# Performance work log

Hardware: AMD Instinct MI355X
Metric: run time of the kernel (lower is better)

## Reference

```python
import jax, jax.numpy as jnp
import numpy as np

B, L, N, D = 16, 4096, 512, 256
EPS = 1e-8  # torch F.cosine_similarity default eps


def setup_inputs() -> dict:
    key = jax.random.key(0)
    k1, k2, k3 = jax.random.split(key, 3)
    spk_decoder_out = jax.random.normal(k1, (B, L, D), dtype=jnp.float32)
    profile = jax.random.normal(k2, (B, N, D), dtype=jnp.float32)
    # lengths in [1, N] so every batch has at least one valid profile
    profile_lens = jax.random.randint(k3, (B,), 1, N + 1, dtype=jnp.int32)
    return {"spk_decoder_out": spk_decoder_out, "profile": profile,
            "profile_lens": profile_lens}


def reference(spk_decoder_out, profile, profile_lens):
    # cosine similarity between (B,L,1,D) and (B,1,N,D) along D, computed
    # without materializing the (B,L,N,D) broadcast intermediate
    dots = jnp.einsum('bld,bnd->bln', spk_decoder_out, profile)      # (B,L,N)
    x_norm = jnp.sqrt(jnp.sum(spk_decoder_out * spk_decoder_out, axis=-1))  # (B,L)
    p_norm = jnp.sqrt(jnp.sum(profile * profile, axis=-1))           # (B,N)
    denom = jnp.maximum(x_norm[:, :, None] * p_norm[:, None, :], EPS)
    sim = dots / denom                                               # (B,L,N)

    # pad mask over profiles: True where n >= profile_lens[b]
    n = profile.shape[1]
    mask = jnp.arange(n, dtype=profile_lens.dtype)[None, :] >= profile_lens[:, None]  # (B,N)
    min_value = jnp.finfo(jnp.float32).min
    sim = jnp.where(mask[:, None, :], min_value, sim)
    weights = jax.nn.softmax(sim, axis=-1)
    weights = jnp.where(mask[:, None, :], 0.0, weights)              # (B,L,N)

    spk_embedding = jnp.einsum('bln,bnd->bld', weights, profile)     # (B,L,D)
    return spk_embedding, weights
```

## Files before the change

kernel.cpp:

```cpp
#include <hip/hip_runtime.h>
#include <hip/hip_bf16.h>
#include <math.h>

#define BB 16
#define LL 4096
#define NN 512
#define DD 256

typedef __attribute__((ext_vector_type(8))) short  bf16x8;
typedef __attribute__((ext_vector_type(4))) float  f32x4;
typedef __attribute__((ext_vector_type(4))) unsigned short u16x4;
typedef __attribute__((ext_vector_type(8))) unsigned short u16x8;

typedef __attribute__((address_space(1))) const void  gvoid_t;
typedef __attribute__((address_space(3))) void        lvoid_t;

#define GLL16(src, dst) __builtin_amdgcn_global_load_lds((gvoid_t*)(src), (lvoid_t*)(dst), 16, 0, 0)

__device__ __forceinline__ unsigned short f2bf(float x) {
    union { float f; unsigned u; } v; v.f = x;
    unsigned r = v.u + 0x7fffu + ((v.u >> 16) & 1u);
    return (unsigned short)(r >> 16);
}
__device__ __forceinline__ float bfhi(unsigned u) { return __uint_as_float(u & 0xffff0000u); }
__device__ __forceinline__ float bflo(unsigned u) { return __uint_as_float(u << 16); }

__global__ __launch_bounds__(256) void cda_prep(
    const float* __restrict__ P, char* __restrict__ pnI, char* __restrict__ peI)
{
    __shared__ __align__(16) char raw[16384];

    const int blk = blockIdx.x;
    const int b   = blk >> 4;
    const int c   = blk & 15;
    const int tid = threadIdx.x;
    const int nl  = tid >> 3;
    const int sub = tid & 7;

    const float* rowp = P + (((size_t)b * NN + c * 32 + nl) * DD + sub * 32);
    float4 v[8];
    #pragma unroll
    for (int k = 0; k < 8; ++k) v[k] = *(const float4*)(rowp + k * 4);

    float ss = 0.f;
    #pragma unroll
    for (int k = 0; k < 8; ++k)
        ss += v[k].x * v[k].x + v[k].y * v[k].y + v[k].z * v[k].z + v[k].w * v[k].w;
    ss += __shfl_xor(ss, 1); ss += __shfl_xor(ss, 2); ss += __shfl_xor(ss, 4);
    const float rinv = 1.0f / sqrtf(ss);

    const size_t tile = ((size_t)b * 16 + c) * 16384;

    #pragma unroll
    for (int g = 0; g < 4; ++g) {
        u16x8 h;
        #pragma unroll
        for (int j = 0; j < 8; ++j) {
            const int dl = g * 8 + j;
            const float f = ((const float*)&v[dl >> 2])[dl & 3];
            h[j] = f2bf(f * rinv);
        }
        *(u16x8*)(pnI + tile + sub * 2048 + (nl >> 4) * 1024 + (g * 16 + (nl & 15)) * 16) = h;
    }

    #pragma unroll
    for (int g = 0; g < 4; ++g) {
        u16x8 h;
        #pragma unroll
        for (int j = 0; j < 8; ++j) {
            const int dl = g * 8 + j;
            h[j] = f2bf(((const float*)&v[dl >> 2])[dl & 3]);
        }
        *(u16x8*)(raw + ((nl * 512 + sub * 64 + g * 16) ^ ((nl & 7) << 4))) = h;
    }
    __syncthreads();

    unsigned short arr[32];
    #pragma unroll
    for (int r = 0; r < 32; ++r)
        arr[r] = *(const unsigned short*)(raw + ((r * 512 + tid * 2) ^ ((r & 7) << 4)));
    #pragma unroll
    for (int g = 0; g < 4; ++g) {
        u16x8 h;
        #pragma unroll
        for (int j = 0; j < 8; ++j)
            h[j] = arr[g * 4 + (j & 3) + 16 * (j >> 2)];
        *(u16x8*)(peI + tile + (tid >> 4) * 1024 + (g * 16 + (tid & 15)) * 16) = h;
    }
}

__global__ __launch_bounds__(256, 2) void cda_main(
    const float* __restrict__ X, const char* __restrict__ pnI,
    const char* __restrict__ peI, const int* __restrict__ lens,
    float* __restrict__ out)
{
    __shared__ __align__(16) char stg[65536];

    const int id = blockIdx.x;
    const int b  = (id & 7) * 2 + (id >> 9);
    const int l0 = ((id >> 3) & 63) * 64;

    const int tid  = threadIdx.x;
    const int w    = tid >> 6;
    const int lane = tid & 63;
    const int lo   = lane & 15;
    const int g    = lane >> 4;
    const int len  = lens[b];

    const float* Xb  = X + ((size_t)b * LL + l0) * DD;
    const char*  pnB = pnI + (size_t)b * 262144;
    const char*  peB = peI + (size_t)b * 262144;

    #pragma unroll
    for (int q = 0; q < 4; ++q)
        GLL16(pnB + q * 4096 + tid * 16, stg + q * 4096 + tid * 16);

    float xinv = 0.f;
    #pragma unroll
    for (int rr = 0; rr < 16; ++rr) {
        const int row = w * 16 + rr;
        const float4 v = *(const float4*)(Xb + row * DD + lane * 4);
        float ss = v.x * v.x + v.y * v.y + v.z * v.z + v.w * v.w;
        #pragma unroll
        for (int off = 32; off > 0; off >>= 1) ss += __shfl_xor(ss, off);
        const float inv = 1.0f / sqrtf(ss);
        if (rr == lo) xinv = inv;
        u16x4 h; h.x = f2bf(v.x); h.y = f2bf(v.y); h.z = f2bf(v.z); h.w = f2bf(v.w);
        *(u16x4*)(stg + 16384 + ((row * 512 + lane * 8) ^ ((row & 7) << 4))) = h;
    }
    __syncthreads();
    bf16x8 xf[8];
    #pragma unroll
    for (int ks = 0; ks < 8; ++ks)
        xf[ks] = *(const bf16x8*)(stg + 16384 +
            (((w * 16 + lo) * 512 + ks * 64 + g * 16) ^ ((lo & 7) << 4)));
    __syncthreads();

    #pragma unroll
    for (int q = 0; q < 4; ++q)
        GLL16(pnB + 16384 + q * 4096 + tid * 16, stg + 16384 + q * 4096 + tid * 16);
    #pragma unroll
    for (int q = 0; q < 4; ++q)
        GLL16(pnB + 32768 + q * 4096 + tid * 16, stg + 32768 + q * 4096 + tid * 16);

    unsigned pm[16][4];
    float ssum = 0.f;

    #pragma unroll
    for (int c = 0; c < 16; ++c) {
        asm volatile("s_waitcnt vmcnt(8)" ::: "memory");
        __builtin_amdgcn_s_barrier();
        __builtin_amdgcn_sched_barrier(0);
        {
            const char* src = (c < 13) ? (pnB + (c + 3) * 16384)
                                       : (peB + (c - 13) * 16384);
            char* dst = stg + ((c + 3) & 3) * 16384;
            #pragma unroll
            for (int q = 0; q < 4; ++q)
                GLL16(src + q * 4096 + tid * 16, dst + q * 4096 + tid * 16);
        }
        const char* pnL = stg + (c & 3) * 16384;
        f32x4 a0 = (f32x4){0.f, 0.f, 0.f, 0.f};
        f32x4 a1 = (f32x4){0.f, 0.f, 0.f, 0.f};
        #pragma unroll
        for (int ks = 0; ks < 8; ++ks) {
            const bf16x8 f0 = *(const bf16x8*)(pnL + ks * 2048 + lane * 16);
            const bf16x8 f1 = *(const bf16x8*)(pnL + ks * 2048 + 1024 + lane * 16);
            a0 = __builtin_amdgcn_mfma_f32_16x16x32_bf16(f0, xf[ks], a0, 0, 0, 0);
            a1 = __builtin_amdgcn_mfma_f32_16x16x32_bf16(f1, xf[ks], a1, 0, 0, 0);
        }
        unsigned short pw[8];
        #pragma unroll
        for (int r = 0; r < 4; ++r) {
            const int n0 = c * 32 + g * 4 + r;
            const float p0 = (n0 < len) ? __expf(a0[r] * xinv) : 0.f;
            ssum += p0; pw[r] = f2bf(p0);
            const float p1 = (n0 + 16 < len) ? __expf(a1[r] * xinv) : 0.f;
            ssum += p1; pw[4 + r] = f2bf(p1);
        }
        pm[c][0] = (unsigned)pw[0] | ((unsigned)pw[1] << 16);
        pm[c][1] = (unsigned)pw[2] | ((unsigned)pw[3] << 16);
        pm[c][2] = (unsigned)pw[4] | ((unsigned)pw[5] << 16);
        pm[c][3] = (unsigned)pw[6] | ((unsigned)pw[7] << 16);
    }

    ssum += __shfl_xor(ssum, 16);
    ssum += __shfl_xor(ssum, 32);
    const float sinv = 1.0f / ssum;

    f32x4 e[16];
    #pragma unroll
    for (int i = 0; i < 16; ++i) e[i] = (f32x4){0.f, 0.f, 0.f, 0.f};

    float* Wrow = out + (size_t)BB * LL * DD
                + ((size_t)b * LL + l0 + w * 16 + lo) * (size_t)NN;

    #pragma unroll
    for (int c = 0; c < 16; ++c) {
        if      (c == 0) asm volatile("s_waitcnt vmcnt(8)"  ::: "memory");
        else if (c == 1) asm volatile("s_waitcnt vmcnt(10)" ::: "memory");
        else if (c <= 13) asm volatile("s_waitcnt vmcnt(12)" ::: "memory");
        else if (c == 14) asm volatile("s_waitcnt vmcnt(8)"  ::: "memory");
        else             asm volatile("s_waitcnt vmcnt(4)"  ::: "memory");
        __builtin_amdgcn_s_barrier();
        __builtin_amdgcn_sched_barrier(0);
        if (c < 13) {
            const char* src = peB + (c + 3) * 16384;
            char* dst = stg + ((c + 3) & 3) * 16384;
            #pragma unroll
            for (int q = 0; q < 4; ++q)
                GLL16(src + q * 4096 + tid * 16, dst + q * 4096 + tid * 16);
        }
        float4 v0, v1;
        v0.x = bflo(pm[c][0]) * sinv; v0.y = bfhi(pm[c][0]) * sinv;
        v0.z = bflo(pm[c][1]) * sinv; v0.w = bfhi(pm[c][1]) * sinv;
        v1.x = bflo(pm[c][2]) * sinv; v1.y = bfhi(pm[c][2]) * sinv;
        v1.z = bflo(pm[c][3]) * sinv; v1.w = bfhi(pm[c][3]) * sinv;
        *(float4*)(Wrow + c * 32 + g * 4)      = v0;
        *(float4*)(Wrow + c * 32 + 16 + g * 4) = v1;

        union { unsigned u[4]; bf16x8 v; } pf;
        pf.u[0] = pm[c][0]; pf.u[1] = pm[c][1];
        pf.u[2] = pm[c][2]; pf.u[3] = pm[c][3];
        const char* peL = stg + (c & 3) * 16384;
        #pragma unroll
        for (int df = 0; df < 16; ++df) {
            const bf16x8 bf = *(const bf16x8*)(peL + df * 1024 + lane * 16);
            e[df] = __builtin_amdgcn_mfma_f32_16x16x32_bf16(pf.v, bf, e[df], 0, 0, 0);
        }
    }
    __syncthreads();

    float t4[4];
    #pragma unroll
    for (int r = 0; r < 4; ++r) t4[r] = __shfl(sinv, g * 4 + r);
    char* scr = stg + w * 16384;
    float* Eout = out + ((size_t)b * LL + l0 + w * 16) * DD;
    #pragma unroll
    for (int r = 0; r < 4; ++r) {
        #pragma unroll
        for (int df = 0; df < 16; ++df)
            *(float*)(scr + g * 1056 + df * 64 + lo * 4) = e[df][r] * t4[r];
        #pragma unroll
        for (int it = 0; it < 4; ++it) {
            const float4 t = *(const float4*)(scr + it * 1056 + lane * 16);
            *(float4*)(Eout + (size_t)(it * 4 + r) * DD + lane * 4) = t;
        }
    }
}

extern "C" void kernel_launch(void* const* d_in, const int* in_sizes, int n_in,
                              void* d_out, int out_size, void* d_ws, size_t ws_size,
                              hipStream_t stream) {
    const float* X    = (const float*)d_in[0];
    const float* P    = (const float*)d_in[1];
    const int*   lens = (const int*)d_in[2];
    float*       out  = (float*)d_out;

    char* pnI = (char*)d_ws;
    char* peI = (char*)d_ws + 4194304;

    hipLaunchKernelGGL(cda_prep, dim3(BB * 16), dim3(256), 0, stream, P, pnI, peI);
    hipLaunchKernelGGL(cda_main, dim3(1024), dim3(256), 0, stream, X, pnI, peI, lens, out);
}
```

Baseline: 82.05 us.

## Software-pipeline softmax exp behind next chunk MFMAs, add setprio and nontemporal stores

The exp/convert work for chunk c-1 of the similarity scores now runs after the MFMAs for chunk c are issued, so the transcendental ALU work can overlap matrix-core latency. MFMA blocks are wrapped in s_setprio raises so waves doing matrix math get issue priority. Output stores for weights and embeddings switch to nontemporal stores to avoid polluting cache with write-once data. This holds an extra pair of accumulators live, which raises register pressure.

```diff
diff --git a/kernel.cpp b/kernel.cpp
--- a/kernel.cpp
+++ b/kernel.cpp
@@ -146,6 +146,8 @@
     unsigned pm[16][4];
     float ssum = 0.f;
 
+    f32x4 a0p = (f32x4){0.f, 0.f, 0.f, 0.f};
+    f32x4 a1p = (f32x4){0.f, 0.f, 0.f, 0.f};
     #pragma unroll
     for (int c = 0; c < 16; ++c) {
         asm volatile("s_waitcnt vmcnt(8)" ::: "memory");
@@ -162,6 +164,7 @@
         const char* pnL = stg + (c & 3) * 16384;
         f32x4 a0 = (f32x4){0.f, 0.f, 0.f, 0.f};
         f32x4 a1 = (f32x4){0.f, 0.f, 0.f, 0.f};
+        __builtin_amdgcn_s_setprio(1);
         #pragma unroll
         for (int ks = 0; ks < 8; ++ks) {
             const bf16x8 f0 = *(const bf16x8*)(pnL + ks * 2048 + lane * 16);
@@ -169,19 +172,39 @@
             a0 = __builtin_amdgcn_mfma_f32_16x16x32_bf16(f0, xf[ks], a0, 0, 0, 0);
             a1 = __builtin_amdgcn_mfma_f32_16x16x32_bf16(f1, xf[ks], a1, 0, 0, 0);
         }
+        __builtin_amdgcn_s_setprio(0);
+        if (c > 0) {
+            const int cp = c - 1;
+            unsigned short pw[8];
+            #pragma unroll
+            for (int r = 0; r < 4; ++r) {
+                const int n0 = cp * 32 + g * 4 + r;
+                const float p0 = (n0 < len) ? __expf(a0p[r] * xinv) : 0.f;
+                ssum += p0; pw[r] = f2bf(p0);
+                const float p1 = (n0 + 16 < len) ? __expf(a1p[r] * xinv) : 0.f;
+                ssum += p1; pw[4 + r] = f2bf(p1);
+            }
+            pm[cp][0] = (unsigned)pw[0] | ((unsigned)pw[1] << 16);
+            pm[cp][1] = (unsigned)pw[2] | ((unsigned)pw[3] << 16);
+            pm[cp][2] = (unsigned)pw[4] | ((unsigned)pw[5] << 16);
+            pm[cp][3] = (unsigned)pw[6] | ((unsigned)pw[7] << 16);
+        }
+        a0p = a0; a1p = a1;
+    }
+    {
         unsigned short pw[8];
         #pragma unroll
         for (int r = 0; r < 4; ++r) {
-            const int n0 = c * 32 + g * 4 + r;
-            const float p0 = (n0 < len) ? __expf(a0[r] * xinv) : 0.f;
+            const int n0 = 15 * 32 + g * 4 + r;
+            const float p0 = (n0 < len) ? __expf(a0p[r] * xinv) : 0.f;
             ssum += p0; pw[r] = f2bf(p0);
-            const float p1 = (n0 + 16 < len) ? __expf(a1[r] * xinv) : 0.f;
+            const float p1 = (n0 + 16 < len) ? __expf(a1p[r] * xinv) : 0.f;
             ssum += p1; pw[4 + r] = f2bf(p1);
         }
-        pm[c][0] = (unsigned)pw[0] | ((unsigned)pw[1] << 16);
-        pm[c][1] = (unsigned)pw[2] | ((unsigned)pw[3] << 16);
-        pm[c][2] = (unsigned)pw[4] | ((unsigned)pw[5] << 16);
-        pm[c][3] = (unsigned)pw[6] | ((unsigned)pw[7] << 16);
+        pm[15][0] = (unsigned)pw[0] | ((unsigned)pw[1] << 16);
+        pm[15][1] = (unsigned)pw[2] | ((unsigned)pw[3] << 16);
+        pm[15][2] = (unsigned)pw[4] | ((unsigned)pw[5] << 16);
+        pm[15][3] = (unsigned)pw[6] | ((unsigned)pw[7] << 16);
     }
 
     ssum += __shfl_xor(ssum, 16);
@@ -211,23 +234,25 @@
             for (int q = 0; q < 4; ++q)
                 GLL16(src + q * 4096 + tid * 16, dst + q * 4096 + tid * 16);
         }
-        float4 v0, v1;
-        v0.x = bflo(pm[c][0]) * sinv; v0.y = bfhi(pm[c][0]) * sinv;
-        v0.z = bflo(pm[c][1]) * sinv; v0.w = bfhi(pm[c][1]) * sinv;
-        v1.x = bflo(pm[c][2]) * sinv; v1.y = bfhi(pm[c][2]) * sinv;
-        v1.z = bflo(pm[c][3]) * sinv; v1.w = bfhi(pm[c][3]) * sinv;
-        *(float4*)(Wrow + c * 32 + g * 4)      = v0;
-        *(float4*)(Wrow + c * 32 + 16 + g * 4) = v1;
+        f32x4 v0, v1;
+        v0[0] = bflo(pm[c][0]) * sinv; v0[1] = bfhi(pm[c][0]) * sinv;
+        v0[2] = bflo(pm[c][1]) * sinv; v0[3] = bfhi(pm[c][1]) * sinv;
+        v1[0] = bflo(pm[c][2]) * sinv; v1[1] = bfhi(pm[c][2]) * sinv;
+        v1[2] = bflo(pm[c][3]) * sinv; v1[3] = bfhi(pm[c][3]) * sinv;
+        __builtin_nontemporal_store(v0, (f32x4*)(Wrow + c * 32 + g * 4));
+        __builtin_nontemporal_store(v1, (f32x4*)(Wrow + c * 32 + 16 + g * 4));
 
         union { unsigned u[4]; bf16x8 v; } pf;
         pf.u[0] = pm[c][0]; pf.u[1] = pm[c][1];
         pf.u[2] = pm[c][2]; pf.u[3] = pm[c][3];
         const char* peL = stg + (c & 3) * 16384;
+        __builtin_amdgcn_s_setprio(1);
         #pragma unroll
         for (int df = 0; df < 16; ++df) {
             const bf16x8 bf = *(const bf16x8*)(peL + df * 1024 + lane * 16);
             e[df] = __builtin_amdgcn_mfma_f32_16x16x32_bf16(pf.v, bf, e[df], 0, 0, 0);
         }
+        __builtin_amdgcn_s_setprio(0);
     }
     __syncthreads();
 
@@ -243,8 +268,8 @@
             *(float*)(scr + g * 1056 + df * 64 + lo * 4) = e[df][r] * t4[r];
         #pragma unroll
         for (int it = 0; it < 4; ++it) {
-            const float4 t = *(const float4*)(scr + it * 1056 + lane * 16);
-            *(float4*)(Eout + (size_t)(it * 4 + r) * DD + lane * 4) = t;
+            const f32x4 t = *(const f32x4*)(scr + it * 1056 + lane * 16);
+            __builtin_nontemporal_store(t, (f32x4*)(Eout + (size_t)(it * 4 + r) * DD + lane * 4));
         }
     }
 }
```

After: 83.87 us. +2.2%, slower.

## Split PV matmul across warps by D columns, sharing P tiles via LDS

Applied to the files above, without the earlier changes.

Each warp now exchanges its bf16 probability fragment through a small LDS buffer so that every warp computes all 64 rows of the block for its own 64-column slice of D. Previously each warp computed its own 16 rows across all 256 columns. Each warp now reads only a quarter of the staged profile tile from LDS per chunk, cutting LDS bandwidth for the B operand. The cost is an extra LDS write and block barrier per chunk, plus an epilogue rewritten around a per-row scale table.

```diff
diff --git a/kernel.cpp b/kernel.cpp
--- a/kernel.cpp
+++ b/kernel.cpp
@@ -95,6 +95,8 @@
     float* __restrict__ out)
 {
     __shared__ __align__(16) char stg[65536];
+    __shared__ __align__(16) char pmat[4096];
+    __shared__ float tbl[64];
 
     const int id = blockIdx.x;
     const int b  = (id & 7) * 2 + (id >> 9);
@@ -187,6 +189,7 @@
     ssum += __shfl_xor(ssum, 16);
     ssum += __shfl_xor(ssum, 32);
     const float sinv = 1.0f / ssum;
+    if (lane < 16) tbl[w * 16 + lane] = sinv;
 
     f32x4 e[16];
     #pragma unroll
@@ -219,32 +222,51 @@
         *(float4*)(Wrow + c * 32 + g * 4)      = v0;
         *(float4*)(Wrow + c * 32 + 16 + g * 4) = v1;
 
-        union { unsigned u[4]; bf16x8 v; } pf;
+        union { unsigned u[4]; bf16x8 v; u16x8 h; } pf;
         pf.u[0] = pm[c][0]; pf.u[1] = pm[c][1];
         pf.u[2] = pm[c][2]; pf.u[3] = pm[c][3];
+        *(u16x8*)(pmat + w * 1024 + lane * 16) = pf.h;
+        asm volatile("s_waitcnt lgkmcnt(0)" ::: "memory");
+        __builtin_amdgcn_s_barrier();
+        __builtin_amdgcn_sched_barrier(0);
+
         const char* peL = stg + (c & 3) * 16384;
         #pragma unroll
-        for (int df = 0; df < 16; ++df) {
-            const bf16x8 bf = *(const bf16x8*)(peL + df * 1024 + lane * 16);
-            e[df] = __builtin_amdgcn_mfma_f32_16x16x32_bf16(pf.v, bf, e[df], 0, 0, 0);
-        }
-    }
-    __syncthreads();
-
-    float t4[4];
-    #pragma unroll
-    for (int r = 0; r < 4; ++r) t4[r] = __shfl(sinv, g * 4 + r);
-    char* scr = stg + w * 16384;
-    float* Eout = out + ((size_t)b * LL + l0 + w * 16) * DD;
-    #pragma unroll
-    for (int r = 0; r < 4; ++r) {
-        #pragma unroll
-        for (int df = 0; df < 16; ++df)
-            *(float*)(scr + g * 1056 + df * 64 + lo * 4) = e[df][r] * t4[r];
-        #pragma unroll
-        for (int it = 0; it < 4; ++it) {
-            const float4 t = *(const float4*)(scr + it * 1056 + lane * 16);
-            *(float4*)(Eout + (size_t)(it * 4 + r) * DD + lane * 4) = t;
+        for (int m = 0; m < 4; ++m) {
+            bf16x8 af;
+            if (m == w) af = pf.v;
+            else        af = *(const bf16x8*)(pmat + m * 1024 + lane * 16);
+            #pragma unroll
+            for (int df = 0; df < 4; ++df) {
+                const bf16x8 bf = *(const bf16x8*)(peL + (w * 4 + df) * 1024 + lane * 16);
+                e[m * 4 + df] = __builtin_amdgcn_mfma_f32_16x16x32_bf16(af, bf, e[m * 4 + df], 0, 0, 0);
+            }
+        }
+    }
+    __syncthreads();
+
+    char* scr = stg + w * 8448;
+    float* EoutW = out + ((size_t)b * LL + l0) * DD + w * 64;
+    #pragma unroll
+    for (int h = 0; h < 2; ++h) {
+        #pragma unroll
+        for (int mm = 0; mm < 2; ++mm) {
+            const int m = h * 2 + mm;
+            #pragma unroll
+            for (int r = 0; r < 4; ++r) {
+                const int rl = mm * 16 + g * 4 + r;
+                const float sv = tbl[h * 32 + rl];
+                #pragma unroll
+                for (int df = 0; df < 4; ++df)
+                    *(float*)(scr + rl * 260 + (df * 16 + lo) * 4) = e[m * 4 + df][r] * sv;
+            }
+        }
+        #pragma unroll
+        for (int it = 0; it < 8; ++it) {
+            const int rl   = it * 4 + (lane >> 4);
+            const int colq = lane & 15;
+            const float4 t = *(const float4*)(scr + rl * 260 + colq * 16);
+            *(float4*)(EoutW + (size_t)(h * 32 + rl) * DD + colq * 4) = t;
         }
     }
 }
```

Measured after the change: 90.24 us. 10.0% more time.

## Fuse P·V accumulation into score loop with double-buffered pn/pe staging

Applied to the files above, without the earlier changes.

Moves the weights×profile MFMA accumulation into the same chunk loop that computes similarity scores. Each iteration stages both the normalized-profile and embedding chunk into a two-slot double buffer, replacing the separate four-deep ring for each pass. This removes the second pipelined pass and its drain, and interleaves exp work with MFMA work. In exchange, prefetch depth drops to one chunk with full barriers, and the e accumulators stay live through the score loop, which raises register pressure.

```diff
diff --git a/kernel.cpp b/kernel.cpp
--- a/kernel.cpp
+++ b/kernel.cpp
@@ -114,6 +114,9 @@
     #pragma unroll
     for (int q = 0; q < 4; ++q)
         GLL16(pnB + q * 4096 + tid * 16, stg + q * 4096 + tid * 16);
+    #pragma unroll
+    for (int q = 0; q < 4; ++q)
+        GLL16(peB + q * 4096 + tid * 16, stg + 16384 + q * 4096 + tid * 16);
 
     float xinv = 0.f;
     #pragma unroll
@@ -126,40 +129,45 @@
         const float inv = 1.0f / sqrtf(ss);
         if (rr == lo) xinv = inv;
         u16x4 h; h.x = f2bf(v.x); h.y = f2bf(v.y); h.z = f2bf(v.z); h.w = f2bf(v.w);
-        *(u16x4*)(stg + 16384 + ((row * 512 + lane * 8) ^ ((row & 7) << 4))) = h;
+        *(u16x4*)(stg + 32768 + ((row * 512 + lane * 8) ^ ((row & 7) << 4))) = h;
     }
     __syncthreads();
     bf16x8 xf[8];
     #pragma unroll
     for (int ks = 0; ks < 8; ++ks)
-        xf[ks] = *(const bf16x8*)(stg + 16384 +
+        xf[ks] = *(const bf16x8*)(stg + 32768 +
             (((w * 16 + lo) * 512 + ks * 64 + g * 16) ^ ((lo & 7) << 4)));
     __syncthreads();
 
     #pragma unroll
     for (int q = 0; q < 4; ++q)
-        GLL16(pnB + 16384 + q * 4096 + tid * 16, stg + 16384 + q * 4096 + tid * 16);
-    #pragma unroll
-    for (int q = 0; q < 4; ++q)
-        GLL16(pnB + 32768 + q * 4096 + tid * 16, stg + 32768 + q * 4096 + tid * 16);
+        GLL16(pnB + 16384 + q * 4096 + tid * 16, stg + 32768 + q * 4096 + tid * 16);
+    #pragma unroll
+    for (int q = 0; q < 4; ++q)
+        GLL16(peB + 16384 + q * 4096 + tid * 16, stg + 49152 + q * 4096 + tid * 16);
 
     unsigned pm[16][4];
     float ssum = 0.f;
+    f32x4 e[16];
+    #pragma unroll
+    for (int i = 0; i < 16; ++i) e[i] = (f32x4){0.f, 0.f, 0.f, 0.f};
 
     #pragma unroll
     for (int c = 0; c < 16; ++c) {
-        asm volatile("s_waitcnt vmcnt(8)" ::: "memory");
-        __builtin_amdgcn_s_barrier();
-        __builtin_amdgcn_sched_barrier(0);
-        {
-            const char* src = (c < 13) ? (pnB + (c + 3) * 16384)
-                                       : (peB + (c - 13) * 16384);
-            char* dst = stg + ((c + 3) & 3) * 16384;
+        __syncthreads();
+        if (c >= 1 && c < 15) {
+            const char* srcn = pnB + (size_t)(c + 1) * 16384;
+            const char* srce = peB + (size_t)(c + 1) * 16384;
+            char* dst = stg + ((c + 1) & 1) * 32768;
             #pragma unroll
             for (int q = 0; q < 4; ++q)
-                GLL16(src + q * 4096 + tid * 16, dst + q * 4096 + tid * 16);
-        }
-        const char* pnL = stg + (c & 3) * 16384;
+                GLL16(srcn + q * 4096 + tid * 16, dst + q * 4096 + tid * 16);
+            #pragma unroll
+            for (int q = 0; q < 4; ++q)
+                GLL16(srce + q * 4096 + tid * 16, dst + 16384 + q * 4096 + tid * 16);
+        }
+        const char* pnL = stg + (c & 1) * 32768;
+
         f32x4 a0 = (f32x4){0.f, 0.f, 0.f, 0.f};
         f32x4 a1 = (f32x4){0.f, 0.f, 0.f, 0.f};
         #pragma unroll
@@ -182,35 +190,45 @@
         pm[c][1] = (unsigned)pw[2] | ((unsigned)pw[3] << 16);
         pm[c][2] = (unsigned)pw[4] | ((unsigned)pw[5] << 16);
         pm[c][3] = (unsigned)pw[6] | ((unsigned)pw[7] << 16);
+
+        union { unsigned u[4]; bf16x8 v; } pf;
+        pf.u[0] = pm[c][0]; pf.u[1] = pm[c][1];
+        pf.u[2] = pm[c][2]; pf.u[3] = pm[c][3];
+        const char* peL = pnL + 16384;
+        #pragma unroll
+        for (int df = 0; df < 16; ++df) {
+            const bf16x8 bf = *(const bf16x8*)(peL + df * 1024 + lane * 16);
+            e[df] = __builtin_amdgcn_mfma_f32_16x16x32_bf16(pf.v, bf, e[df], 0, 0, 0);
+        }
     }
 
     ssum += __shfl_xor(ssum, 16);
     ssum += __shfl_xor(ssum, 32);
     const float sinv = 1.0f / ssum;
 
-    f32x4 e[16];
-    #pragma unroll
-    for (int i = 0; i < 16; ++i) e[i] = (f32x4){0.f, 0.f, 0.f, 0.f};
+    __syncthreads();
+
+    float t4[4];
+    #pragma unroll
+    for (int r = 0; r < 4; ++r) t4[r] = __shfl(sinv, g * 4 + r);
+    char* scr = stg + w * 16384;
+    float* Eout = out + ((size_t)b * LL + l0 + w * 16) * DD;
+    #pragma unroll
+    for (int r = 0; r < 4; ++r) {
+        #pragma unroll
+        for (int df = 0; df < 16; ++df)
+            *(float*)(scr + g * 1056 + df * 64 + lo * 4) = e[df][r] * t4[r];
+        #pragma unroll
+        for (int it = 0; it < 4; ++it) {
+            const float4 t = *(const float4*)(scr + it * 1056 + lane * 16);
+            *(float4*)(Eout + (size_t)(it * 4 + r) * DD + lane * 4) = t;
+        }
+    }
 
     float* Wrow = out + (size_t)BB * LL * DD
                 + ((size_t)b * LL + l0 + w * 16 + lo) * (size_t)NN;
-
     #pragma unroll
     for (int c = 0; c < 16; ++c) {
-        if      (c == 0) asm volatile("s_waitcnt vmcnt(8)"  ::: "memory");
-        else if (c == 1) asm volatile("s_waitcnt vmcnt(10)" ::: "memory");
-        else if (c <= 13) asm volatile("s_waitcnt vmcnt(12)" ::: "memory");
-        else if (c == 14) asm volatile("s_waitcnt vmcnt(8)"  ::: "memory");
-        else             asm volatile("s_waitcnt vmcnt(4)"  ::: "memory");
-        __builtin_amdgcn_s_barrier();
-        __builtin_amdgcn_sched_barrier(0);
-        if (c < 13) {
-            const char* src = peB + (c + 3) * 16384;
-            char* dst = stg + ((c + 3) & 3) * 16384;
-            #pragma unroll
-            for (int q = 0; q < 4; ++q)
-                GLL16(src + q * 4096 + tid * 16, dst + q * 4096 + tid * 16);
-        }
         float4 v0, v1;
         v0.x = bflo(pm[c][0]) * sinv; v0.y = bfhi(pm[c][0]) * sinv;
         v0.z = bflo(pm[c][1]) * sinv; v0.w = bfhi(pm[c][1]) * sinv;
@@ -218,34 +236,6 @@
         v1.z = bflo(pm[c][3]) * sinv; v1.w = bfhi(pm[c][3]) * sinv;
         *(float4*)(Wrow + c * 32 + g * 4)      = v0;
         *(float4*)(Wrow + c * 32 + 16 + g * 4) = v1;
-
-        union { unsigned u[4]; bf16x8 v; } pf;
-        pf.u[0] = pm[c][0]; pf.u[1] = pm[c][1];
-        pf.u[2] = pm[c][2]; pf.u[3] = pm[c][3];
-        const char* peL = stg + (c & 3) * 16384;
-        #pragma unroll
-        for (int df = 0; df < 16; ++df) {
-            const bf16x8 bf = *(const bf16x8*)(peL + df * 1024 + lane * 16);
-            e[df] = __builtin_amdgcn_mfma_f32_16x16x32_bf16(pf.v, bf, e[df], 0, 0, 0);
-        }
-    }
-    __syncthreads();
-
-    float t4[4];
-    #pragma unroll
-    for (int r = 0; r < 4; ++r) t4[r] = __shfl(sinv, g * 4 + r);
-    char* scr = stg + w * 16384;
-    float* Eout = out + ((size_t)b * LL + l0 + w * 16) * DD;
-    #pragma unroll
-    for (int r = 0; r < 4; ++r) {
-        #pragma unroll
-        for (int df = 0; df < 16; ++df)
-            *(float*)(scr + g * 1056 + df * 64 + lo * 4) = e[df][r] * t4[r];
-        #pragma unroll
-        for (int it = 0; it < 4; ++it) {
-            const float4 t = *(const float4*)(scr + it * 1056 + lane * 16);
-            *(float4*)(Eout + (size_t)(it * 4 + r) * DD + lane * 4) = t;
-        }
     }
 }
 
```

After: 145.0 us. 1.77x slower.
